# Kernel tuning notes

Hardware: AMD Instinct MI355X
Metric: run time of the kernel (lower is better)

## Reference

```python
import jax, jax.numpy as jnp
import numpy as np

B, N, MODES, WIDTH = 4, 8192, 12, 32
TWO = 2 * MODES  # 24
M_TOT = TWO * (TWO - 1)  # 552


def setup_inputs() -> dict:
    key = jax.random.key(0)
    ks = jax.random.split(key, 12)
    scale = 1.0 / (WIDTH * WIDTH)
    x = jax.random.uniform(ks[0], (B, N, 2), jnp.float32)
    fc0_w = jax.random.normal(ks[1], (2, WIDTH), jnp.float32) * 0.1
    fc0_b = jax.random.normal(ks[2], (WIDTH,), jnp.float32) * 0.05
    # 4 layers x {weights1, weights2}, stored as real/imag pairs (torch.rand cfloat ~ U[0,1)+1j*U[0,1))
    spec_w = jax.random.uniform(ks[3], (4, 2, WIDTH, WIDTH, MODES, MODES, 2), jnp.float32) * scale
    conv_w = jax.random.normal(ks[4], (4, WIDTH, WIDTH), jnp.float32) * 0.1  # Conv1d k=1 -> [O,I]
    conv_b = jax.random.normal(ks[5], (4, WIDTH), jnp.float32) * 0.05
    fc1_w = jax.random.normal(ks[6], (WIDTH, 128), jnp.float32) * 0.1
    fc1_b = jax.random.normal(ks[7], (128,), jnp.float32) * 0.05
    fc2_w = jax.random.normal(ks[8], (128, 1), jnp.float32) * 0.1
    fc2_b = jax.random.normal(ks[9], (1,), jnp.float32) * 0.05
    return {"x": x, "fc0_w": fc0_w, "fc0_b": fc0_b, "spec_w": spec_w,
            "conv_w": conv_w, "conv_b": conv_b, "fc1_w": fc1_w, "fc1_b": fc1_b,
            "fc2_w": fc2_w, "fc2_b": fc2_b}


def _vft_matrices(xp, yp):
    # xp, yp: [B, N], already min-shifted and scaled to [0, 6.28]
    kx = jnp.concatenate([jnp.arange(MODES), jnp.arange(-MODES, 0)]).astype(jnp.float32)       # [24]
    ky = jnp.concatenate([jnp.arange(MODES), jnp.arange(-(MODES - 1), 0)]).astype(jnp.float32)  # [23]
    Xm = kx[None, :, None] * xp[:, None, :]  # [B,24,N]
    Ym = ky[None, :, None] * yp[:, None, :]  # [B,23,N]
    # torch: X repeat(1,23,1) tiles blocks; Y repeat(1,1,24).reshape interleaves -> row j*24+i = X[i]+Y[j]
    phase = jnp.tile(Xm, (1, TWO - 1, 1)) + jnp.repeat(Ym, TWO, axis=1)  # [B,552,N]
    V_fwd = jnp.exp(-1j * phase)                    # [B,552,N] complex64
    V_inv = jnp.conj(V_fwd).transpose(0, 2, 1)      # [B,N,552]
    return V_fwd, V_inv


def _spectral_conv(h, V_fwd, V_inv, w1, w2):
    # h: [B,C,N] real; w1,w2: [C,C,M,M] complex
    b, c, n = h.shape
    # forward Vandermonde transform: bmm(V_fwd, h^T) then permute -> [B,C,552]
    x_ft = jnp.einsum('bmn,bnc->bcm', V_fwd, h.astype(jnp.complex64).transpose(0, 2, 1))
    x_ft = x_ft.reshape(b, c, TWO, TWO - 1)
    top = jnp.einsum('bixy,ioxy->boxy', x_ft[:, :, :MODES, :MODES], w1)
    bot = jnp.einsum('bixy,ioxy->boxy', x_ft[:, :, -MODES:, :MODES], w2)
    out_ft = jnp.zeros((b, WIDTH, TWO, MODES), jnp.complex64)
    out_ft = out_ft.at[:, :, :MODES, :MODES].set(top)
    out_ft = out_ft.at[:, :, -MODES:, :MODES].set(bot)
    x_ft = out_ft.reshape(b, WIDTH, 2 * MODES * MODES)  # [B,C,288]
    # conjugate-symmetric completion (flip over last two dims, as in source)
    x_ft2 = jnp.conj(jnp.flip(x_ft[..., TWO:], axis=(-2, -1)))  # [B,C,264]
    x_ft = jnp.concatenate([x_ft, x_ft2], axis=-1)  # [B,C,552]
    out = jnp.einsum('bnm,bmc->bcn', V_inv, x_ft.transpose(0, 2, 1))  # [B,C,N]
    return (out / n * 2).real


def reference(x, fc0_w, fc0_b, spec_w, conv_w, conv_b, fc1_w, fc1_b, fc2_w, fc2_b):
    gelu = lambda t: jax.nn.gelu(t, approximate=False)
    # VFT mutates x in-place by subtracting global mins (view semantics in torch)
    xp = x[:, :, 0] - jnp.min(x[:, :, 0])
    yp = x[:, :, 1] - jnp.min(x[:, :, 1])
    x_in = jnp.stack([xp, yp], axis=-1)  # what fc0 actually sees
    V_fwd, V_inv = _vft_matrices(xp * 6.28 / jnp.max(xp), yp * 6.28 / jnp.max(yp))
    h = (x_in @ fc0_w + fc0_b).transpose(0, 2, 1)  # [B,C,N]
    for l in range(4):
        w1 = spec_w[l, 0, ..., 0] + 1j * spec_w[l, 0, ..., 1]
        w2 = spec_w[l, 1, ..., 0] + 1j * spec_w[l, 1, ..., 1]
        x1 = _spectral_conv(h, V_fwd, V_inv, w1, w2)
        x2 = jnp.einsum('bin,oi->bon', h, conv_w[l]) + conv_b[l][None, :, None]
        h = x1 + x2
        if l < 3:
            h = gelu(h)
    h = h.transpose(0, 2, 1)  # [B,N,C]
    h = gelu(h @ fc1_w + fc1_b)
    return h @ fc2_w + fc2_b  # [B,N,1]
```

## Files before the change

kernel.cpp:

```cpp
#include <hip/hip_runtime.h>
#include <cmath>

#define NB 4
#define NN 8192
#define CH 32

typedef short short8 __attribute__((ext_vector_type(8)));
typedef float floatx4 __attribute__((ext_vector_type(4)));
typedef unsigned short ushort_t;

__device__ __forceinline__ unsigned short f2b(float f){
  unsigned u = __float_as_uint(f);
  u = u + 0x7FFFu + ((u >> 16) & 1u);
  return (unsigned short)(u >> 16);
}
__device__ __forceinline__ float b2f(unsigned short h){
  return __uint_as_float(((unsigned)h) << 16);
}
__device__ __forceinline__ float gelu_f(float v){
  return 0.5f * v * (1.0f + erff(v * 0.70710678118654752440f));
}
__device__ __forceinline__ int repk(int t){
  int j = t / 24, i = t - j * 24;
  if(j == 0)  return (i <= 12) ? i : -1;
  if(j <= 11) return 13 + (j - 1) * 24 + i;
  return (i == 12) ? 277 + (j - 12) : -1;
}
__device__ __forceinline__ int partner(int t){
  int j = t / 24, i = t - j * 24;
  return ((23 - j) % 23) * 24 + ((24 - i) % 24);
}
__device__ __forceinline__ int repT(int k){
  if(k < 13) return k;
  if(k < 277){ int m = k - 13; return (m / 24 + 1) * 24 + (m % 24); }
  return (k - 277 + 12) * 24 + 12;
}

__global__ __launch_bounds__(256) void k_pre(const float* __restrict__ spec,
    float2* __restrict__ wt, const float* __restrict__ x, float4* __restrict__ pmm)
{
  const int tid = threadIdx.x;
  if(blockIdx.x < 128){
    int g = blockIdx.x * 256 + tid;
    float a = x[(size_t)g * 2], b = x[(size_t)g * 2 + 1];
    float mn0 = a, mx0 = a, mn1 = b, mx1 = b;
    for(int off = 32; off > 0; off >>= 1){
      mn0 = fminf(mn0, __shfl_down(mn0, off));
      mx0 = fmaxf(mx0, __shfl_down(mx0, off));
      mn1 = fminf(mn1, __shfl_down(mn1, off));
      mx1 = fmaxf(mx1, __shfl_down(mx1, off));
    }
    __shared__ float4 wp[4];
    if((tid & 63) == 0) wp[tid >> 6] = make_float4(mn0, mn1, mx0, mx1);
    __syncthreads();
    if(tid == 0){
      float4 r = wp[0];
      for(int i2 = 1; i2 < 4; ++i2){
        float4 v = wp[i2];
        r.x = fminf(r.x, v.x); r.y = fminf(r.y, v.y);
        r.z = fmaxf(r.z, v.z); r.w = fmaxf(r.w, v.w);
      }
      pmm[blockIdx.x] = r;
    }
  } else {
    int g = (blockIdx.x - 128) * 256 + tid;
    int o  = g & 31;
    int i  = (g >> 5) & 31;
    int rest = g >> 10;
    int pq = rest % 144;
    int ls = rest / 144;
    wt[g] = ((const float2*)spec)[(((size_t)(ls * 32 + i) * 32 + o) * 144 + pq)];
  }
}

__global__ __launch_bounds__(256) void k_vbuild(const float* __restrict__ x,
    const float4* __restrict__ pmm, const float* __restrict__ fw,
    const float* __restrict__ fb, ushort_t* __restrict__ AF, ushort_t* __restrict__ VTF,
    float* __restrict__ h, ushort_t* __restrict__ hb)
{
  __shared__ ushort_t lds1[32 * 584];
  __shared__ float4 mmv;
  const int tid = threadIdx.x;
  if(tid < 64){
    float4 a = pmm[tid], c = pmm[tid + 64];
    float mn0 = fminf(a.x, c.x), mn1 = fminf(a.y, c.y);
    float mx0 = fmaxf(a.z, c.z), mx1 = fmaxf(a.w, c.w);
    for(int off = 32; off > 0; off >>= 1){
      mn0 = fminf(mn0, __shfl_down(mn0, off));
      mn1 = fminf(mn1, __shfl_down(mn1, off));
      mx0 = fmaxf(mx0, __shfl_down(mx0, off));
      mx1 = fmaxf(mx1, __shfl_down(mx1, off));
    }
    if(tid == 0) mmv = make_float4(mn0, mn1, mx0, mx1);
  }
  __syncthreads();
  const int nl = tid & 31, part = tid >> 5;
  const int b = blockIdx.x >> 8;
  const int nblk = blockIdx.x & 255;
  const int n = nblk * 32 + nl;
  float mn0 = mmv.x, mn1 = mmv.y, mx0 = mmv.z, mx1 = mmv.w;
  float x0 = x[(size_t)(b * NN + n) * 2]     - mn0;
  float x1 = x[(size_t)(b * NN + n) * 2 + 1] - mn1;
  float sp = x0 * (6.28f / (mx0 - mn0));
  float sq = x1 * (6.28f / (mx1 - mn1));
  float cx, sx, cy, sy;
  sincosf(sp, &sx, &cx);
  sincosf(sq, &sy, &cy);
  int j0 = part * 3;
  int j1 = (j0 + 3 < 23) ? j0 + 3 : 23;
  float ky0 = (j0 < 12) ? (float)j0 : (float)(j0 - 23);
  float cb, sb;
  sincosf(ky0 * sq, &sb, &cb);
  for(int j = j0; j < j1; ++j){
    float ca = 1.0f, sa = 0.0f;
    #pragma unroll
    for(int i = 0; i < 24; ++i){
      float vr = ca * cb - sa * sb;
      float vi = -(sa * cb + ca * sb);
      int t = j * 24 + i;
      int k = repk(t);
      if(k >= 0){
        lds1[nl * 584 + k]       = f2b(vr);
        lds1[nl * 584 + 288 + k] = f2b(vi);
      }
      float cn = ca * cx - sa * sx;
      float sn = sa * cx + ca * sx;
      if(i == 11) sn = -sn;
      ca = cn; sa = sn;
    }
    float cbn = cb * cy - sb * sy;
    float sbn = sb * cy + cb * sy;
    cb = cbn; sb = sbn;
  }
  __syncthreads();
  #pragma unroll
  for(int r = 0; r < 9; ++r){
    int c = tid + 256 * r;
    int t16 = c / 1152;
    int c2 = c - t16 * 1152;
    int kk = c2 >> 6;
    int rem = c2 & 63;
    int q = rem >> 4, n15 = rem & 15;
    short8 v = *(const short8*)(lds1 + (t16 * 16 + n15) * 584 + kk * 32 + q * 8);
    *(short8*)(VTF + ((size_t)((b * 512 + nblk * 2 + t16) * 18 + kk)) * 512
               + (q * 16 + n15) * 8) = v;
  }
  #pragma unroll
  for(int r = 0; r < 9; ++r){
    int c = tid + 256 * r;
    int st = c >> 6;
    int rem = c & 63;
    int q = rem >> 4, srow = rem & 15;
    int sg = st * 16 + srow;
    int s = (sg < 288) ? sg : sg - 288;
    int sinh_ = (sg >= 288);
    int p2 = s / 12, qq = s - p2 * 12;
    int t = p2 * 23 + qq;
    int k = repk(t);
    unsigned short flip = 0;
    if(k < 0){ k = repk(partner(t)); if(sinh_) flip = 0x8000; }
    int col = sinh_ ? 288 + k : k;
    ushort_t tmp[8];
    #pragma unroll
    for(int e = 0; e < 8; ++e)
      tmp[e] = lds1[(q * 8 + e) * 584 + col] ^ flip;
    *(short8*)(AF + ((size_t)((b * 36 + st) * 256 + nblk)) * 512
               + (q * 16 + srow) * 8) = *(short8*)tmp;
  }
  #pragma unroll
  for(int rr = 0; rr < 4; ++rr){
    int c2 = (tid >> 5) + rr * 8;
    float v = fb[c2] + x0 * fw[c2] + x1 * fw[32 + c2];
    size_t idx = (size_t)(b * CH + c2) * NN + n;
    h[idx] = v; hb[idx] = f2b(v);
  }
}

__global__ __launch_bounds__(256) void k_fwd(const ushort_t* __restrict__ AF,
    const ushort_t* __restrict__ hb, float* __restrict__ xp)
{
  const int stp = blockIdx.x;
  const int ks = blockIdx.y;
  const int b  = blockIdx.z;
  const int w = threadIdx.x >> 6;
  const int lane = threadIdx.x & 63;
  const int row = lane & 15;
  const int q = lane >> 4;
  const int st0 = stp * 2;
  const size_t abase0 = ((size_t)(b * 36 + st0) * 256) * 512 + (q * 16 + row) * 8;
  const size_t abase1 = abase0 + (size_t)256 * 512;
  const size_t hb0 = (size_t)(b * CH + row) * NN;
  const size_t hb1 = hb0 + (size_t)16 * NN;
  floatx4 aA0 = {0.f,0.f,0.f,0.f}, aA1 = {0.f,0.f,0.f,0.f};
  floatx4 aB0 = {0.f,0.f,0.f,0.f}, aB1 = {0.f,0.f,0.f,0.f};
  #pragma unroll
  for(int kk = 0; kk < 8; ++kk){
    int g = ks * 32 + w * 8 + kk;
    short8 A0 = *(const short8*)(AF + abase0 + (size_t)g * 512);
    short8 A1 = *(const short8*)(AF + abase1 + (size_t)g * 512);
    int nn2 = g * 32 + q * 8;
    short8 B0 = *(const short8*)(hb + hb0 + nn2);
    short8 B1 = *(const short8*)(hb + hb1 + nn2);
    aA0 = __builtin_amdgcn_mfma_f32_16x16x32_bf16(A0, B0, aA0, 0, 0, 0);
    aA1 = __builtin_amdgcn_mfma_f32_16x16x32_bf16(A0, B1, aA1, 0, 0, 0);
    aB0 = __builtin_amdgcn_mfma_f32_16x16x32_bf16(A1, B0, aB0, 0, 0, 0);
    aB1 = __builtin_amdgcn_mfma_f32_16x16x32_bf16(A1, B1, aB1, 0, 0, 0);
  }
  __shared__ float red[4 * 512];
  const int e = threadIdx.x;
  #pragma unroll
  for(int r = 0; r < 4; ++r){
    int rrow = q * 4 + r;
    red[w * 512 + rrow * 32 + row]      = aA0[r];
    red[w * 512 + rrow * 32 + 16 + row] = aA1[r];
  }
  __syncthreads();
  {
    float v0 = red[e] + red[512 + e] + red[1024 + e] + red[1536 + e];
    float v1 = red[e + 256] + red[512 + e + 256] + red[1024 + e + 256] + red[1536 + e + 256];
    size_t base = ((size_t)(ks * NB + b) * 576 + st0 * 16) * 32;
    xp[base + e] = v0;
    xp[base + e + 256] = v1;
  }
  __syncthreads();
  #pragma unroll
  for(int r = 0; r < 4; ++r){
    int rrow = q * 4 + r;
    red[w * 512 + rrow * 32 + row]      = aB0[r];
    red[w * 512 + rrow * 32 + 16 + row] = aB1[r];
  }
  __syncthreads();
  {
    float v0 = red[e] + red[512 + e] + red[1024 + e] + red[1536 + e];
    float v1 = red[e + 256] + red[512 + e + 256] + red[1024 + e + 256] + red[1536 + e + 256];
    size_t base = ((size_t)(ks * NB + b) * 576 + (st0 + 1) * 16) * 32;
    xp[base + e] = v0;
    xp[base + e + 256] = v1;
  }
}

__global__ __launch_bounds__(256) void k_mixg(const float* __restrict__ xp,
    const float2* __restrict__ wt, ushort_t* __restrict__ ghi, ushort_t* __restrict__ glo,
    int layer)
{
  const int w = threadIdx.x >> 6;
  const int lane = threadIdx.x & 63;
  const int k = blockIdx.x * 4 + w;
  const int b = blockIdx.y;
  const int t = repT(k);
  const int j = t / 24, i = t - j * 24;
  const int u = partner(t);
  const bool unpaired = (i == 12) || (u == t);
  const int idxT = (t < 288) ? t : 575 - t;  const bool cfT = (t >= 288);
  const int idxU = (u < 288) ? u : 575 - u;  const bool cfU = (u >= 288);
  __shared__ float Xs[4][2][64];
  const int o = lane & 31, half = lane >> 5;
  #pragma unroll
  for(int m = 0; m < 2; ++m){
    int idx = m ? idxU : idxT;
    int rrow = half ? 288 + idx : idx;
    float s = 0.f;
    #pragma unroll
    for(int ks = 0; ks < 8; ++ks)
      s += xp[((size_t)(ks * NB + b) * 576 + rrow) * 32 + o];
    Xs[w][m][half * 32 + o] = s;
  }
  __syncthreads();
  float Fr[2], Fi[2];
  #pragma unroll
  for(int m = 0; m < 2; ++m){
    int idx = m ? idxU : idxT;
    int p2 = idx / 12, qq = idx - p2 * 12;
    int sel = (p2 < 12) ? 0 : 1;
    int pq = (p2 % 12) * 12 + qq;
    const float2* wb = wt + ((size_t)((layer * 2 + sel) * 144 + pq)) * 1024;
    int i0 = half * 16;
    float fr = 0.f, fi = 0.f;
    #pragma unroll
    for(int ii = 0; ii < 16; ++ii){
      int i2 = i0 + ii;
      float xr = Xs[w][m][i2], xi = Xs[w][m][32 + i2];
      float2 wv = wb[i2 * 32 + o];
      fr += xr * wv.x - xi * wv.y;
      fi += xr * wv.y + xi * wv.x;
    }
    fr += __shfl_down(fr, 32);
    fi += __shfl_down(fi, 32);
    Fr[m] = fr; Fi[m] = fi;
  }
  const int c = lane & 31;
  const int srcT = cfT ? 31 - c : c;
  const int srcU = cfU ? 31 - c : c;
  float fax = __shfl(Fr[0], srcT);
  float fay = __shfl(Fi[0], srcT);
  float fbx = __shfl(Fr[1], srcU);
  float fby = __shfl(Fi[1], srcU);
  if(lane < 32){
    float gr = fax;
    float gi = cfT ? -fay : fay;
    if(!unpaired){
      gr += fbx;
      gi -= (cfU ? -fby : fby);
    }
    unsigned short hr = f2b(gr); float lr = gr - b2f(hr);
    unsigned short hi2 = f2b(gi); float li = gi - b2f(hi2);
    size_t base = (size_t)(b * CH + c) * 576;
    ghi[base + k] = hr;          ghi[base + 288 + k] = hi2;
    glo[base + k] = f2b(lr);     glo[base + 288 + k] = f2b(li);
  }
}

template<int LAST>
__global__ __launch_bounds__(512, 2) void k_inv(const ushort_t* __restrict__ VTF,
    const ushort_t* __restrict__ ghi, const ushort_t* __restrict__ glo,
    const float* __restrict__ hfull, const float* __restrict__ cw,
    const float* __restrict__ cbias, float* __restrict__ hout,
    ushort_t* __restrict__ houtb, int layer,
    const float* __restrict__ w1, const float* __restrict__ b1,
    const float* __restrict__ w2, const float* __restrict__ b2,
    float* __restrict__ out)
{
  __shared__ ushort_t GH[32][584];
  __shared__ ushort_t GL[32][584];
  __shared__ float hTc[32][129];
  __shared__ float Wl[1024];
  __shared__ float Bl[32];
  const int tid = threadIdx.x;
  const int b = blockIdx.y;
  const int n0 = blockIdx.x * 128;
  for(int idx = tid; idx < 2304; idx += 512){
    int ch = idx / 72, g8 = (idx - ch * 72) * 8;
    size_t src = (size_t)(b * CH + ch) * 576 + g8;
    *(short8*)&GH[ch][g8] = *(const short8*)(ghi + src);
    *(short8*)&GL[ch][g8] = *(const short8*)(glo + src);
  }
  {
    int ch = tid >> 4, grp = tid & 15;
    const float* src = hfull + (size_t)(b * CH + ch) * NN + n0 + grp * 8;
    float4 v0 = *(const float4*)src;
    float4 v1 = *(const float4*)(src + 4);
    int p = grp * 8;
    hTc[ch][p + 0] = v0.x; hTc[ch][p + 1] = v0.y;
    hTc[ch][p + 2] = v0.z; hTc[ch][p + 3] = v0.w;
    hTc[ch][p + 4] = v1.x; hTc[ch][p + 5] = v1.y;
    hTc[ch][p + 6] = v1.z; hTc[ch][p + 7] = v1.w;
  }
  for(int idx = tid; idx < 1024; idx += 512)
    Wl[(idx & 31) * 32 + (idx >> 5)] = cw[layer * 1024 + idx];
  if(tid < 32) Bl[tid] = cbias[layer * 32 + tid];
  __syncthreads();
  const int lane = tid & 63;
  const int w = tid >> 6;
  const int row = lane & 15;
  const int q = lane >> 4;
  const int nloc = w * 16 + row;
  const int n = n0 + nloc;
  const int n16 = blockIdx.x * 8 + w;
  const ushort_t* vb = VTF + ((size_t)(b * 512 + n16) * 18) * 512 + (q * 16 + row) * 8;
  const int ko = q * 8;
  floatx4 acc0 = {0.f,0.f,0.f,0.f}, acc1 = {0.f,0.f,0.f,0.f};
  #pragma unroll
  for(int kk = 0; kk < 18; ++kk){
    short8 Bv  = *(const short8*)(vb + (size_t)kk * 512);
    short8 Ah0 = *(const short8*)&GH[row][ko + kk * 32];
    short8 Al0 = *(const short8*)&GL[row][ko + kk * 32];
    short8 Ah1 = *(const short8*)&GH[16 + row][ko + kk * 32];
    short8 Al1 = *(const short8*)&GL[16 + row][ko + kk * 32];
    acc0 = __builtin_amdgcn_mfma_f32_16x16x32_bf16(Ah0, Bv, acc0, 0, 0, 0);
    acc0 = __builtin_amdgcn_mfma_f32_16x16x32_bf16(Al0, Bv, acc0, 0, 0, 0);
    acc1 = __builtin_amdgcn_mfma_f32_16x16x32_bf16(Ah1, Bv, acc1, 0, 0, 0);
    acc1 = __builtin_amdgcn_mfma_f32_16x16x32_bf16(Al1, Bv, acc1, 0, 0, 0);
  }
  float acc2[8];
  {
    const int c0 = q * 4;
    #pragma unroll
    for(int r = 0; r < 4; ++r){ acc2[r] = Bl[c0 + r]; acc2[4 + r] = Bl[16 + c0 + r]; }
    #pragma unroll
    for(int i = 0; i < CH; ++i){
      float hv = hTc[i][nloc];
      float4 wv0 = *(const float4*)&Wl[i * 32 + c0];
      float4 wv1 = *(const float4*)&Wl[i * 32 + 16 + c0];
      acc2[0] = fmaf(hv, wv0.x, acc2[0]);
      acc2[1] = fmaf(hv, wv0.y, acc2[1]);
      acc2[2] = fmaf(hv, wv0.z, acc2[2]);
      acc2[3] = fmaf(hv, wv0.w, acc2[3]);
      acc2[4] = fmaf(hv, wv1.x, acc2[4]);
      acc2[5] = fmaf(hv, wv1.y, acc2[5]);
      acc2[6] = fmaf(hv, wv1.z, acc2[6]);
      acc2[7] = fmaf(hv, wv1.w, acc2[7]);
    }
  }
  const float sc = 2.0f / 8192.0f;
  if constexpr(!LAST){
    #pragma unroll
    for(int r = 0; r < 4; ++r){
      int c = q * 4 + r;
      float v0 = gelu_f(acc0[r] * sc + acc2[r]);
      size_t idx0 = (size_t)(b * CH + c) * NN + n;
      hout[idx0] = v0; houtb[idx0] = f2b(v0);
      float v1 = gelu_f(acc1[r] * sc + acc2[4 + r]);
      size_t idx1 = (size_t)(b * CH + 16 + c) * NN + n;
      hout[idx1] = v1; houtb[idx1] = f2b(v1);
    }
  } else {
    __shared__ float hT2[128][33];
    __shared__ float Wfc1[4096];
    __shared__ float b1s[128], w2s[128];
    __shared__ float red2[512];
    #pragma unroll
    for(int r = 0; r < 4; ++r){
      int c = q * 4 + r;
      hT2[nloc][c]      = acc0[r] * sc + acc2[r];
      hT2[nloc][16 + c] = acc1[r] * sc + acc2[4 + r];
    }
    for(int idx2 = tid; idx2 < 4096; idx2 += 512) Wfc1[idx2] = w1[idx2];
    if(tid < 128){ b1s[tid] = b1[tid]; w2s[tid] = w2[tid]; }
    __syncthreads();
    const int nl2 = tid & 127;
    const int js = tid >> 7;
    float acc3 = 0.f;
    for(int jj = js * 32; jj < js * 32 + 32; ++jj){
      float s = b1s[jj];
      #pragma unroll
      for(int i = 0; i < CH; ++i) s = fmaf(hT2[nl2][i], Wfc1[i * 128 + jj], s);
      acc3 = fmaf(gelu_f(s), w2s[jj], acc3);
    }
    red2[tid] = acc3;
    __syncthreads();
    if(js == 0){
      float v = red2[nl2] + red2[nl2 + 128] + red2[nl2 + 256] + red2[nl2 + 384] + b2[0];
      out[(size_t)b * NN + n0 + nl2] = v;
    }
  }
}

extern "C" void kernel_launch(void* const* d_in, const int* in_sizes, int n_in,
                              void* d_out, int out_size, void* d_ws, size_t ws_size,
                              hipStream_t stream)
{
  const float* x      = (const float*)d_in[0];
  const float* fc0_w  = (const float*)d_in[1];
  const float* fc0_b  = (const float*)d_in[2];
  const float* spec_w = (const float*)d_in[3];
  const float* conv_w = (const float*)d_in[4];
  const float* conv_b = (const float*)d_in[5];
  const float* fc1_w  = (const float*)d_in[6];
  const float* fc1_b  = (const float*)d_in[7];
  const float* fc2_w  = (const float*)d_in[8];
  const float* fc2_b  = (const float*)d_in[9];
  float* out = (float*)d_out;

  char* w = (char*)d_ws;
  const size_t OFF_PMM  = 0;
  const size_t OFF_WT   = 4096;
  const size_t OFF_AF   = OFF_WT  + 9437184;
  const size_t OFF_VTF  = OFF_AF  + 37748736;
  const size_t OFF_H0   = OFF_VTF + 37748736;
  const size_t OFF_H1   = OFF_H0  + 4194304;
  const size_t OFF_H0B  = OFF_H1  + 4194304;
  const size_t OFF_H1B  = OFF_H0B + 2097152;
  const size_t OFF_XP   = OFF_H1B + 2097152;
  const size_t OFF_GHI  = OFF_XP  + 2359296;
  const size_t OFF_GLO  = OFF_GHI + 147456;

  float4* pmm    = (float4*)(w + OFF_PMM);
  float2* wt     = (float2*)(w + OFF_WT);
  ushort_t* AF   = (ushort_t*)(w + OFF_AF);
  ushort_t* VTF  = (ushort_t*)(w + OFF_VTF);
  float* hbuf[2]     = { (float*)(w + OFF_H0), (float*)(w + OFF_H1) };
  ushort_t* hbufb[2] = { (ushort_t*)(w + OFF_H0B), (ushort_t*)(w + OFF_H1B) };
  float* xp      = (float*)(w + OFF_XP);
  ushort_t* ghi  = (ushort_t*)(w + OFF_GHI);
  ushort_t* glo  = (ushort_t*)(w + OFF_GLO);

  hipLaunchKernelGGL(k_pre, dim3(4736), dim3(256), 0, stream, spec_w, wt, x, pmm);
  hipLaunchKernelGGL(k_vbuild, dim3(1024), dim3(256), 0, stream, x, pmm,
                     fc0_w, fc0_b, AF, VTF, hbuf[0], hbufb[0]);

  for(int l = 0; l < 4; ++l){
    int in = l & 1, outb = 1 - in;
    hipLaunchKernelGGL(k_fwd, dim3(18, 8, NB), dim3(256), 0, stream, AF, hbufb[in], xp);
    hipLaunchKernelGGL(k_mixg, dim3(72, NB), dim3(256), 0, stream, xp, wt, ghi, glo, l);
    if(l < 3)
      hipLaunchKernelGGL(k_inv<0>, dim3(64, NB), dim3(512), 0, stream, VTF, ghi, glo,
                         hbuf[in], conv_w, conv_b, hbuf[outb], hbufb[outb], l,
                         fc1_w, fc1_b, fc2_w, fc2_b, out);
    else
      hipLaunchKernelGGL(k_inv<1>, dim3(64, NB), dim3(512), 0, stream, VTF, ghi, glo,
                         hbuf[in], conv_w, conv_b, hbuf[outb], hbufb[outb], l,
                         fc1_w, fc1_b, fc2_w, fc2_b, out);
  }
  (void)in_sizes; (void)n_in; (void)out_size; (void)ws_size;
}
```

Baseline: 256.2 us.

## Split k_fwd K-range finer, prefetch MFMA operands, fold weight transpose into vbuild

k_fwd's K dimension is split into 16 slices instead of 8, doubling grid parallelism, and all A/B operands are loaded up front before the MFMA chain. k_mixg now sums 16 partial slices, and the xp workspace is doubled to match. k_inv prefetches its 18 VTF fragments into registers before the LDS staging and barrier so global latency overlaps that setup. The spectral weight transpose moves from k_pre into k_vbuild as a grid-stride loop, so k_pre shrinks to the min/max reduction. The costs are more partial-sum traffic and higher register pressure in k_inv.

```diff
diff --git a/kernel.cpp b/kernel.cpp
--- a/kernel.cpp
+++ b/kernel.cpp
@@ -36,47 +36,37 @@
   return (k - 277 + 12) * 24 + 12;
 }
 
-__global__ __launch_bounds__(256) void k_pre(const float* __restrict__ spec,
-    float2* __restrict__ wt, const float* __restrict__ x, float4* __restrict__ pmm)
+__global__ __launch_bounds__(256) void k_pre(const float* __restrict__ x, float4* __restrict__ pmm)
 {
   const int tid = threadIdx.x;
-  if(blockIdx.x < 128){
-    int g = blockIdx.x * 256 + tid;
-    float a = x[(size_t)g * 2], b = x[(size_t)g * 2 + 1];
-    float mn0 = a, mx0 = a, mn1 = b, mx1 = b;
-    for(int off = 32; off > 0; off >>= 1){
-      mn0 = fminf(mn0, __shfl_down(mn0, off));
-      mx0 = fmaxf(mx0, __shfl_down(mx0, off));
-      mn1 = fminf(mn1, __shfl_down(mn1, off));
-      mx1 = fmaxf(mx1, __shfl_down(mx1, off));
-    }
-    __shared__ float4 wp[4];
-    if((tid & 63) == 0) wp[tid >> 6] = make_float4(mn0, mn1, mx0, mx1);
-    __syncthreads();
-    if(tid == 0){
-      float4 r = wp[0];
-      for(int i2 = 1; i2 < 4; ++i2){
-        float4 v = wp[i2];
-        r.x = fminf(r.x, v.x); r.y = fminf(r.y, v.y);
-        r.z = fmaxf(r.z, v.z); r.w = fmaxf(r.w, v.w);
-      }
-      pmm[blockIdx.x] = r;
-    }
-  } else {
-    int g = (blockIdx.x - 128) * 256 + tid;
-    int o  = g & 31;
-    int i  = (g >> 5) & 31;
-    int rest = g >> 10;
-    int pq = rest % 144;
-    int ls = rest / 144;
-    wt[g] = ((const float2*)spec)[(((size_t)(ls * 32 + i) * 32 + o) * 144 + pq)];
+  int g = blockIdx.x * 256 + tid;
+  float a = x[(size_t)g * 2], b = x[(size_t)g * 2 + 1];
+  float mn0 = a, mx0 = a, mn1 = b, mx1 = b;
+  for(int off = 32; off > 0; off >>= 1){
+    mn0 = fminf(mn0, __shfl_down(mn0, off));
+    mx0 = fmaxf(mx0, __shfl_down(mx0, off));
+    mn1 = fminf(mn1, __shfl_down(mn1, off));
+    mx1 = fmaxf(mx1, __shfl_down(mx1, off));
+  }
+  __shared__ float4 wp[4];
+  if((tid & 63) == 0) wp[tid >> 6] = make_float4(mn0, mn1, mx0, mx1);
+  __syncthreads();
+  if(tid == 0){
+    float4 r = wp[0];
+    for(int i2 = 1; i2 < 4; ++i2){
+      float4 v = wp[i2];
+      r.x = fminf(r.x, v.x); r.y = fminf(r.y, v.y);
+      r.z = fmaxf(r.z, v.z); r.w = fmaxf(r.w, v.w);
+    }
+    pmm[blockIdx.x] = r;
   }
 }
 
 __global__ __launch_bounds__(256) void k_vbuild(const float* __restrict__ x,
     const float4* __restrict__ pmm, const float* __restrict__ fw,
     const float* __restrict__ fb, ushort_t* __restrict__ AF, ushort_t* __restrict__ VTF,
-    float* __restrict__ h, ushort_t* __restrict__ hb)
+    float* __restrict__ h, ushort_t* __restrict__ hb,
+    const float* __restrict__ spec, float2* __restrict__ wt)
 {
   __shared__ ushort_t lds1[32 * 584];
   __shared__ float4 mmv;
@@ -92,6 +82,14 @@
       mx1 = fmaxf(mx1, __shfl_down(mx1, off));
     }
     if(tid == 0) mmv = make_float4(mn0, mn1, mx0, mx1);
+  }
+  for(int g = blockIdx.x * 256 + tid; g < 1179648; g += 262144){
+    int o  = g & 31;
+    int i  = (g >> 5) & 31;
+    int rest = g >> 10;
+    int pq = rest % 144;
+    int ls = rest / 144;
+    wt[g] = ((const float2*)spec)[(((size_t)(ls * 32 + i) * 32 + o) * 144 + pq)];
   }
   __syncthreads();
   const int nl = tid & 31, part = tid >> 5;
@@ -191,20 +189,24 @@
   const size_t abase1 = abase0 + (size_t)256 * 512;
   const size_t hb0 = (size_t)(b * CH + row) * NN;
   const size_t hb1 = hb0 + (size_t)16 * NN;
+  short8 A0[4], A1[4], B0[4], B1[4];
+  #pragma unroll
+  for(int kk = 0; kk < 4; ++kk){
+    int g = ks * 16 + w * 4 + kk;
+    A0[kk] = *(const short8*)(AF + abase0 + (size_t)g * 512);
+    A1[kk] = *(const short8*)(AF + abase1 + (size_t)g * 512);
+    int nn2 = g * 32 + q * 8;
+    B0[kk] = *(const short8*)(hb + hb0 + nn2);
+    B1[kk] = *(const short8*)(hb + hb1 + nn2);
+  }
   floatx4 aA0 = {0.f,0.f,0.f,0.f}, aA1 = {0.f,0.f,0.f,0.f};
   floatx4 aB0 = {0.f,0.f,0.f,0.f}, aB1 = {0.f,0.f,0.f,0.f};
   #pragma unroll
-  for(int kk = 0; kk < 8; ++kk){
-    int g = ks * 32 + w * 8 + kk;
-    short8 A0 = *(const short8*)(AF + abase0 + (size_t)g * 512);
-    short8 A1 = *(const short8*)(AF + abase1 + (size_t)g * 512);
-    int nn2 = g * 32 + q * 8;
-    short8 B0 = *(const short8*)(hb + hb0 + nn2);
-    short8 B1 = *(const short8*)(hb + hb1 + nn2);
-    aA0 = __builtin_amdgcn_mfma_f32_16x16x32_bf16(A0, B0, aA0, 0, 0, 0);
-    aA1 = __builtin_amdgcn_mfma_f32_16x16x32_bf16(A0, B1, aA1, 0, 0, 0);
-    aB0 = __builtin_amdgcn_mfma_f32_16x16x32_bf16(A1, B0, aB0, 0, 0, 0);
-    aB1 = __builtin_amdgcn_mfma_f32_16x16x32_bf16(A1, B1, aB1, 0, 0, 0);
+  for(int kk = 0; kk < 4; ++kk){
+    aA0 = __builtin_amdgcn_mfma_f32_16x16x32_bf16(A0[kk], B0[kk], aA0, 0, 0, 0);
+    aA1 = __builtin_amdgcn_mfma_f32_16x16x32_bf16(A0[kk], B1[kk], aA1, 0, 0, 0);
+    aB0 = __builtin_amdgcn_mfma_f32_16x16x32_bf16(A1[kk], B0[kk], aB0, 0, 0, 0);
+    aB1 = __builtin_amdgcn_mfma_f32_16x16x32_bf16(A1[kk], B1[kk], aB1, 0, 0, 0);
   }
   __shared__ float red[4 * 512];
   const int e = threadIdx.x;
@@ -261,7 +263,7 @@
     int rrow = half ? 288 + idx : idx;
     float s = 0.f;
     #pragma unroll
-    for(int ks = 0; ks < 8; ++ks)
+    for(int ks = 0; ks < 16; ++ks)
       s += xp[((size_t)(ks * NB + b) * 576 + rrow) * 32 + o];
     Xs[w][m][half * 32 + o] = s;
   }
@@ -328,6 +330,18 @@
   const int tid = threadIdx.x;
   const int b = blockIdx.y;
   const int n0 = blockIdx.x * 128;
+  const int lane = tid & 63;
+  const int w = tid >> 6;
+  const int row = lane & 15;
+  const int q = lane >> 4;
+  const int nloc = w * 16 + row;
+  const int n = n0 + nloc;
+  const int n16 = blockIdx.x * 8 + w;
+  const ushort_t* vb = VTF + ((size_t)(b * 512 + n16) * 18) * 512 + (q * 16 + row) * 8;
+  short8 Bv[18];
+  #pragma unroll
+  for(int kk = 0; kk < 18; ++kk)
+    Bv[kk] = *(const short8*)(vb + (size_t)kk * 512);
   for(int idx = tid; idx < 2304; idx += 512){
     int ch = idx / 72, g8 = (idx - ch * 72) * 8;
     size_t src = (size_t)(b * CH + ch) * 576 + g8;
@@ -349,27 +363,18 @@
     Wl[(idx & 31) * 32 + (idx >> 5)] = cw[layer * 1024 + idx];
   if(tid < 32) Bl[tid] = cbias[layer * 32 + tid];
   __syncthreads();
-  const int lane = tid & 63;
-  const int w = tid >> 6;
-  const int row = lane & 15;
-  const int q = lane >> 4;
-  const int nloc = w * 16 + row;
-  const int n = n0 + nloc;
-  const int n16 = blockIdx.x * 8 + w;
-  const ushort_t* vb = VTF + ((size_t)(b * 512 + n16) * 18) * 512 + (q * 16 + row) * 8;
   const int ko = q * 8;
   floatx4 acc0 = {0.f,0.f,0.f,0.f}, acc1 = {0.f,0.f,0.f,0.f};
   #pragma unroll
   for(int kk = 0; kk < 18; ++kk){
-    short8 Bv  = *(const short8*)(vb + (size_t)kk * 512);
     short8 Ah0 = *(const short8*)&GH[row][ko + kk * 32];
     short8 Al0 = *(const short8*)&GL[row][ko + kk * 32];
     short8 Ah1 = *(const short8*)&GH[16 + row][ko + kk * 32];
     short8 Al1 = *(const short8*)&GL[16 + row][ko + kk * 32];
-    acc0 = __builtin_amdgcn_mfma_f32_16x16x32_bf16(Ah0, Bv, acc0, 0, 0, 0);
-    acc0 = __builtin_amdgcn_mfma_f32_16x16x32_bf16(Al0, Bv, acc0, 0, 0, 0);
-    acc1 = __builtin_amdgcn_mfma_f32_16x16x32_bf16(Ah1, Bv, acc1, 0, 0, 0);
-    acc1 = __builtin_amdgcn_mfma_f32_16x16x32_bf16(Al1, Bv, acc1, 0, 0, 0);
+    acc0 = __builtin_amdgcn_mfma_f32_16x16x32_bf16(Ah0, Bv[kk], acc0, 0, 0, 0);
+    acc0 = __builtin_amdgcn_mfma_f32_16x16x32_bf16(Al0, Bv[kk], acc0, 0, 0, 0);
+    acc1 = __builtin_amdgcn_mfma_f32_16x16x32_bf16(Ah1, Bv[kk], acc1, 0, 0, 0);
+    acc1 = __builtin_amdgcn_mfma_f32_16x16x32_bf16(Al1, Bv[kk], acc1, 0, 0, 0);
   }
   float acc2[8];
   {
@@ -461,7 +466,7 @@
   const size_t OFF_H0B  = OFF_H1  + 4194304;
   const size_t OFF_H1B  = OFF_H0B + 2097152;
   const size_t OFF_XP   = OFF_H1B + 2097152;
-  const size_t OFF_GHI  = OFF_XP  + 2359296;
+  const size_t OFF_GHI  = OFF_XP  + 4718592;
   const size_t OFF_GLO  = OFF_GHI + 147456;
 
   float4* pmm    = (float4*)(w + OFF_PMM);
@@ -474,13 +479,13 @@
   ushort_t* ghi  = (ushort_t*)(w + OFF_GHI);
   ushort_t* glo  = (ushort_t*)(w + OFF_GLO);
 
-  hipLaunchKernelGGL(k_pre, dim3(4736), dim3(256), 0, stream, spec_w, wt, x, pmm);
+  hipLaunchKernelGGL(k_pre, dim3(128), dim3(256), 0, stream, x, pmm);
   hipLaunchKernelGGL(k_vbuild, dim3(1024), dim3(256), 0, stream, x, pmm,
-                     fc0_w, fc0_b, AF, VTF, hbuf[0], hbufb[0]);
+                     fc0_w, fc0_b, AF, VTF, hbuf[0], hbufb[0], spec_w, wt);
 
   for(int l = 0; l < 4; ++l){
     int in = l & 1, outb = 1 - in;
-    hipLaunchKernelGGL(k_fwd, dim3(18, 8, NB), dim3(256), 0, stream, AF, hbufb[in], xp);
+    hipLaunchKernelGGL(k_fwd, dim3(18, 16, NB), dim3(256), 0, stream, AF, hbufb[in], xp);
     hipLaunchKernelGGL(k_mixg, dim3(72, NB), dim3(256), 0, stream, xp, wt, ghi, glo, l);
     if(l < 3)
       hipLaunchKernelGGL(k_inv<0>, dim3(64, NB), dim3(512), 0, stream, VTF, ghi, glo,
```

Measured after the change: 262.7 us. 1.03x slower.

## Fuse spectral mode mixing into inverse kernel with per-batch atomic barrier

Applied to the files above, without the earlier changes.

Removes the separate k_mixg launch. Each k_inv block's waves now compute a slice of the mode-mixing outputs (ghi/glo), bump a per-layer, per-batch atomic counter, and spin until all 64 blocks of that batch have arrived before loading the full spectral coefficients. This saves one kernel launch and its drain gap per layer. In exchange it depends on all 64 blocks per batch being co-resident (a grid-wide spin barrier) and adds the mixing latency to every block's critical path.

```diff
diff --git a/kernel.cpp b/kernel.cpp
--- a/kernel.cpp
+++ b/kernel.cpp
@@ -36,10 +36,77 @@
   return (k - 277 + 12) * 24 + 12;
 }
 
+__device__ __forceinline__ void mixg_wave(const float* __restrict__ xp,
+    const float2* __restrict__ wt, ushort_t* __restrict__ ghi, ushort_t* __restrict__ glo,
+    int layer, int k, int b, int lane, float* Xs )
+{
+  const int t = repT(k);
+  const int j = t / 24, i = t - j * 24;
+  const int u = partner(t);
+  const bool unpaired = (i == 12) || (u == t);
+  const int idxT = (t < 288) ? t : 575 - t;  const bool cfT = (t >= 288);
+  const int idxU = (u < 288) ? u : 575 - u;  const bool cfU = (u >= 288);
+  const int o = lane & 31, half = lane >> 5;
+  #pragma unroll
+  for(int m = 0; m < 2; ++m){
+    int idx = m ? idxU : idxT;
+    int rrow = half ? 288 + idx : idx;
+    float s = 0.f;
+    #pragma unroll
+    for(int ks = 0; ks < 8; ++ks)
+      s += xp[((size_t)(ks * NB + b) * 576 + rrow) * 32 + o];
+    Xs[m * 64 + half * 32 + o] = s;
+  }
+  float Fr[2], Fi[2];
+  #pragma unroll
+  for(int m = 0; m < 2; ++m){
+    int idx = m ? idxU : idxT;
+    int p2 = idx / 12, qq = idx - p2 * 12;
+    int sel = (p2 < 12) ? 0 : 1;
+    int pq = (p2 % 12) * 12 + qq;
+    const float2* wb = wt + ((size_t)((layer * 2 + sel) * 144 + pq)) * 1024;
+    int i0 = half * 16;
+    float fr = 0.f, fi = 0.f;
+    #pragma unroll
+    for(int ii = 0; ii < 16; ++ii){
+      int i2 = i0 + ii;
+      float xr = Xs[m * 64 + i2], xi = Xs[m * 64 + 32 + i2];
+      float2 wv = wb[i2 * 32 + o];
+      fr += xr * wv.x - xi * wv.y;
+      fi += xr * wv.y + xi * wv.x;
+    }
+    fr += __shfl_down(fr, 32);
+    fi += __shfl_down(fi, 32);
+    Fr[m] = fr; Fi[m] = fi;
+  }
+  const int c = lane & 31;
+  const int srcT = cfT ? 31 - c : c;
+  const int srcU = cfU ? 31 - c : c;
+  float fax = __shfl(Fr[0], srcT);
+  float fay = __shfl(Fi[0], srcT);
+  float fbx = __shfl(Fr[1], srcU);
+  float fby = __shfl(Fi[1], srcU);
+  if(lane < 32){
+    float gr = fax;
+    float gi = cfT ? -fay : fay;
+    if(!unpaired){
+      gr += fbx;
+      gi -= (cfU ? -fby : fby);
+    }
+    unsigned short hr = f2b(gr); float lr = gr - b2f(hr);
+    unsigned short hi2 = f2b(gi); float li = gi - b2f(hi2);
+    size_t base = (size_t)(b * CH + c) * 576;
+    ghi[base + k] = hr;          ghi[base + 288 + k] = hi2;
+    glo[base + k] = f2b(lr);     glo[base + 288 + k] = f2b(li);
+  }
+}
+
 __global__ __launch_bounds__(256) void k_pre(const float* __restrict__ spec,
-    float2* __restrict__ wt, const float* __restrict__ x, float4* __restrict__ pmm)
+    float2* __restrict__ wt, const float* __restrict__ x, float4* __restrict__ pmm,
+    int* __restrict__ cnt)
 {
   const int tid = threadIdx.x;
+  if(blockIdx.x == 0 && tid < 16) cnt[tid] = 0;
   if(blockIdx.x < 128){
     int g = blockIdx.x * 256 + tid;
     float a = x[(size_t)g * 2], b = x[(size_t)g * 2 + 1];
@@ -239,101 +306,38 @@
   }
 }
 
-__global__ __launch_bounds__(256) void k_mixg(const float* __restrict__ xp,
-    const float2* __restrict__ wt, ushort_t* __restrict__ ghi, ushort_t* __restrict__ glo,
-    int layer)
-{
-  const int w = threadIdx.x >> 6;
-  const int lane = threadIdx.x & 63;
-  const int k = blockIdx.x * 4 + w;
-  const int b = blockIdx.y;
-  const int t = repT(k);
-  const int j = t / 24, i = t - j * 24;
-  const int u = partner(t);
-  const bool unpaired = (i == 12) || (u == t);
-  const int idxT = (t < 288) ? t : 575 - t;  const bool cfT = (t >= 288);
-  const int idxU = (u < 288) ? u : 575 - u;  const bool cfU = (u >= 288);
-  __shared__ float Xs[4][2][64];
-  const int o = lane & 31, half = lane >> 5;
-  #pragma unroll
-  for(int m = 0; m < 2; ++m){
-    int idx = m ? idxU : idxT;
-    int rrow = half ? 288 + idx : idx;
-    float s = 0.f;
-    #pragma unroll
-    for(int ks = 0; ks < 8; ++ks)
-      s += xp[((size_t)(ks * NB + b) * 576 + rrow) * 32 + o];
-    Xs[w][m][half * 32 + o] = s;
-  }
-  __syncthreads();
-  float Fr[2], Fi[2];
-  #pragma unroll
-  for(int m = 0; m < 2; ++m){
-    int idx = m ? idxU : idxT;
-    int p2 = idx / 12, qq = idx - p2 * 12;
-    int sel = (p2 < 12) ? 0 : 1;
-    int pq = (p2 % 12) * 12 + qq;
-    const float2* wb = wt + ((size_t)((layer * 2 + sel) * 144 + pq)) * 1024;
-    int i0 = half * 16;
-    float fr = 0.f, fi = 0.f;
-    #pragma unroll
-    for(int ii = 0; ii < 16; ++ii){
-      int i2 = i0 + ii;
-      float xr = Xs[w][m][i2], xi = Xs[w][m][32 + i2];
-      float2 wv = wb[i2 * 32 + o];
-      fr += xr * wv.x - xi * wv.y;
-      fi += xr * wv.y + xi * wv.x;
-    }
-    fr += __shfl_down(fr, 32);
-    fi += __shfl_down(fi, 32);
-    Fr[m] = fr; Fi[m] = fi;
-  }
-  const int c = lane & 31;
-  const int srcT = cfT ? 31 - c : c;
-  const int srcU = cfU ? 31 - c : c;
-  float fax = __shfl(Fr[0], srcT);
-  float fay = __shfl(Fi[0], srcT);
-  float fbx = __shfl(Fr[1], srcU);
-  float fby = __shfl(Fi[1], srcU);
-  if(lane < 32){
-    float gr = fax;
-    float gi = cfT ? -fay : fay;
-    if(!unpaired){
-      gr += fbx;
-      gi -= (cfU ? -fby : fby);
-    }
-    unsigned short hr = f2b(gr); float lr = gr - b2f(hr);
-    unsigned short hi2 = f2b(gi); float li = gi - b2f(hi2);
-    size_t base = (size_t)(b * CH + c) * 576;
-    ghi[base + k] = hr;          ghi[base + 288 + k] = hi2;
-    glo[base + k] = f2b(lr);     glo[base + 288 + k] = f2b(li);
-  }
-}
-
 template<int LAST>
 __global__ __launch_bounds__(512, 2) void k_inv(const ushort_t* __restrict__ VTF,
-    const ushort_t* __restrict__ ghi, const ushort_t* __restrict__ glo,
+    ushort_t* __restrict__ ghi, ushort_t* __restrict__ glo,
     const float* __restrict__ hfull, const float* __restrict__ cw,
     const float* __restrict__ cbias, float* __restrict__ hout,
     ushort_t* __restrict__ houtb, int layer,
     const float* __restrict__ w1, const float* __restrict__ b1,
     const float* __restrict__ w2, const float* __restrict__ b2,
-    float* __restrict__ out)
+    float* __restrict__ out,
+    const float* __restrict__ xp, const float2* __restrict__ wt, int* __restrict__ cnt)
 {
   __shared__ ushort_t GH[32][584];
   __shared__ ushort_t GL[32][584];
   __shared__ float hTc[32][129];
   __shared__ float Wl[1024];
   __shared__ float Bl[32];
+  __shared__ float Xsm[8][128];
   const int tid = threadIdx.x;
+  const int bx = blockIdx.x;
   const int b = blockIdx.y;
-  const int n0 = blockIdx.x * 128;
-  for(int idx = tid; idx < 2304; idx += 512){
-    int ch = idx / 72, g8 = (idx - ch * 72) * 8;
-    size_t src = (size_t)(b * CH + ch) * 576 + g8;
-    *(short8*)&GH[ch][g8] = *(const short8*)(ghi + src);
-    *(short8*)&GL[ch][g8] = *(const short8*)(glo + src);
-  }
+  const int n0 = bx * 128;
+  const int lane = tid & 63;
+  const int w = tid >> 6;
+  {
+    int krep = w * 64 + bx;
+    if(krep < 288)
+      mixg_wave(xp, wt, ghi, glo, layer, krep, b, lane, &Xsm[w][0]);
+  }
+  __syncthreads();
+  int* flag = cnt + layer * 4 + b;
+  if(tid == 0)
+    __hip_atomic_fetch_add(flag, 1, __ATOMIC_ACQ_REL, __HIP_MEMORY_SCOPE_AGENT);
   {
     int ch = tid >> 4, grp = tid & 15;
     const float* src = hfull + (size_t)(b * CH + ch) * NN + n0 + grp * 8;
@@ -348,14 +352,23 @@
   for(int idx = tid; idx < 1024; idx += 512)
     Wl[(idx & 31) * 32 + (idx >> 5)] = cw[layer * 1024 + idx];
   if(tid < 32) Bl[tid] = cbias[layer * 32 + tid];
-  __syncthreads();
-  const int lane = tid & 63;
-  const int w = tid >> 6;
+  if(tid == 0){
+    while(__hip_atomic_load(flag, __ATOMIC_ACQUIRE, __HIP_MEMORY_SCOPE_AGENT) < 64)
+      __builtin_amdgcn_s_sleep(2);
+  }
+  __syncthreads();
+  for(int idx = tid; idx < 2304; idx += 512){
+    int ch = idx / 72, g8 = (idx - ch * 72) * 8;
+    size_t src = (size_t)(b * CH + ch) * 576 + g8;
+    *(short8*)&GH[ch][g8] = *(const short8*)(ghi + src);
+    *(short8*)&GL[ch][g8] = *(const short8*)(glo + src);
+  }
+  __syncthreads();
   const int row = lane & 15;
   const int q = lane >> 4;
   const int nloc = w * 16 + row;
   const int n = n0 + nloc;
-  const int n16 = blockIdx.x * 8 + w;
+  const int n16 = bx * 8 + w;
   const ushort_t* vb = VTF + ((size_t)(b * 512 + n16) * 18) * 512 + (q * 16 + row) * 8;
   const int ko = q * 8;
   floatx4 acc0 = {0.f,0.f,0.f,0.f}, acc1 = {0.f,0.f,0.f,0.f};
@@ -453,6 +466,7 @@
 
   char* w = (char*)d_ws;
   const size_t OFF_PMM  = 0;
+  const size_t OFF_CNT  = 2048;
   const size_t OFF_WT   = 4096;
   const size_t OFF_AF   = OFF_WT  + 9437184;
   const size_t OFF_VTF  = OFF_AF  + 37748736;
@@ -465,6 +479,7 @@
   const size_t OFF_GLO  = OFF_GHI + 147456;
 
   float4* pmm    = (float4*)(w + OFF_PMM);
+  int* cnt       = (int*)(w + OFF_CNT);
   float2* wt     = (float2*)(w + OFF_WT);
   ushort_t* AF   = (ushort_t*)(w + OFF_AF);
   ushort_t* VTF  = (ushort_t*)(w + OFF_VTF);
@@ -474,22 +489,21 @@
   ushort_t* ghi  = (ushort_t*)(w + OFF_GHI);
   ushort_t* glo  = (ushort_t*)(w + OFF_GLO);
 
-  hipLaunchKernelGGL(k_pre, dim3(4736), dim3(256), 0, stream, spec_w, wt, x, pmm);
+  hipLaunchKernelGGL(k_pre, dim3(4736), dim3(256), 0, stream, spec_w, wt, x, pmm, cnt);
   hipLaunchKernelGGL(k_vbuild, dim3(1024), dim3(256), 0, stream, x, pmm,
                      fc0_w, fc0_b, AF, VTF, hbuf[0], hbufb[0]);
 
   for(int l = 0; l < 4; ++l){
     int in = l & 1, outb = 1 - in;
     hipLaunchKernelGGL(k_fwd, dim3(18, 8, NB), dim3(256), 0, stream, AF, hbufb[in], xp);
-    hipLaunchKernelGGL(k_mixg, dim3(72, NB), dim3(256), 0, stream, xp, wt, ghi, glo, l);
     if(l < 3)
       hipLaunchKernelGGL(k_inv<0>, dim3(64, NB), dim3(512), 0, stream, VTF, ghi, glo,
                          hbuf[in], conv_w, conv_b, hbuf[outb], hbufb[outb], l,
-                         fc1_w, fc1_b, fc2_w, fc2_b, out);
+                         fc1_w, fc1_b, fc2_w, fc2_b, out, xp, wt, cnt);
     else
       hipLaunchKernelGGL(k_inv<1>, dim3(64, NB), dim3(512), 0, stream, VTF, ghi, glo,
                          hbuf[in], conv_w, conv_b, hbuf[outb], hbufb[outb], l,
-                         fc1_w, fc1_b, fc2_w, fc2_b, out);
+                         fc1_w, fc1_b, fc2_w, fc2_b, out, xp, wt, cnt);
   }
   (void)in_sizes; (void)n_in; (void)out_size; (void)ws_size;
 }
```

After: 303.4 us. 1.18x slower.
